# Kernel optimization log

Hardware: AMD Instinct MI355X
Metric: run time of the kernel (lower is better)

Reference implementation:

```python
import jax, jax.numpy as jnp
import numpy as np

B, N, E, EMB, IN = 8192, 100, 1600, 5, 1
MLP_IN = 50 * 2 * EMB + 50 * 52  # 3100


def _glorot(k, shape):
    fan_in = shape[0]
    return (jax.random.normal(k, shape, jnp.float32) / np.sqrt(fan_in)).astype(jnp.float32)


def setup_inputs() -> dict:
    key = jax.random.key(0)
    ks = jax.random.split(key, 32)
    inp = {
        "data": jax.random.normal(ks[0], (B, N, IN), jnp.float32),
        "d": jax.random.normal(ks[1], (B, 50, 52), jnp.float32),
        "src": jax.random.randint(ks[2], (E,), 0, N, jnp.int32),
        "dst": jax.random.randint(ks[3], (E,), 0, N, jnp.int32),
    }
    # 3 GatedRGCN layers: (1->5), (5->5), (5->5); each has a feature linear W,b and a gate linear G,gb
    dims = [(IN, EMB), (EMB, EMB), (EMB, EMB)]
    for i, (fi, fo) in enumerate(dims):
        inp[f"W{i}"] = _glorot(ks[4 + 4 * i], (fi, fo))
        inp[f"b{i}"] = jnp.zeros((fo,), jnp.float32)
        inp[f"G{i}"] = _glorot(ks[5 + 4 * i], (fo, fo))
        inp[f"gb{i}"] = jnp.zeros((fo,), jnp.float32)
    # MLP head: 3100 -> 128 -> 128 -> 64 -> 2
    mdims = [(MLP_IN, 128), (128, 128), (128, 64), (64, 2)]
    for i, (fi, fo) in enumerate(mdims):
        inp[f"F{i + 1}"] = _glorot(ks[16 + 2 * i], (fi, fo))
        inp[f"fb{i + 1}"] = jnp.zeros((fo,), jnp.float32)
    return inp


def _gated_rgcn_layer(h, src, dst, W, b, G, gb):
    # h: [B, N, F_in]; sum-aggregate neighbor features along edges, then gated linear.
    msgs = h[:, src, :]                                   # [B, E, F_in] gather
    agg = jnp.zeros_like(h).at[:, dst, :].add(msgs)       # [B, N, F_in] scatter-add
    h2 = agg @ W + b                                      # [B, N, F_out]
    gate = jax.nn.sigmoid(h2 @ G + gb)                    # elementwise edge-free gate
    return jax.nn.leaky_relu(gate * h2)                   # LeakyReLU(0.01), torch default


def reference(data, d, src, dst,
              W0, b0, G0, gb0, W1, b1, G1, gb1, W2, b2, G2, gb2,
              F1, fb1, F2, fb2, F3, fb3, F4, fb4):
    x = data
    x = _gated_rgcn_layer(x, src, dst, W0, b0, G0, gb0)
    x = _gated_rgcn_layer(x, src, dst, W1, b1, G1, gb1)
    x = _gated_rgcn_layer(x, src, dst, W2, b2, G2, gb2)
    x = x.reshape(x.shape[0], -1)                         # [B, 500]
    x = jnp.concatenate([x, d.reshape(d.shape[0], -1)], axis=1)  # [B, 3100]
    x = jax.nn.leaky_relu(x @ F1 + fb1)
    x = jax.nn.leaky_relu(x @ F2 + fb2)
    x = jax.nn.leaky_relu(x @ F3 + fb3)
    x = jax.nn.sigmoid(x @ F4 + fb4)                      # [B, 2]
    return x
```

## Files before the change

### kernel.cpp

```cpp
#include <hip/hip_runtime.h>
#include <math.h>

#define NT 256
#define NTG 1024
constexpr int B_   = 8192;
constexpr int N_   = 100;
constexpr int E_   = 1600;
constexpr int EMB  = 5;
constexpr int XDIM = 500;
constexpr int DDIM = 2600;
constexpr int XWP  = 512;
constexpr int DOFF = 512;
constexpr int KPAD = 3136;
constexpr int H1 = 128, H2 = 128, H3 = 64, HO = 2;

typedef short short8 __attribute__((ext_vector_type(8)));
typedef float f32x4  __attribute__((ext_vector_type(4)));

__device__ __forceinline__ float leaky(float v) { return v > 0.f ? v : 0.01f * v; }
__device__ __forceinline__ float sigm(float v)  { return 1.f / (1.f + __expf(-v)); }
__device__ __forceinline__ unsigned short f2bf(float f) {
  unsigned int x = __float_as_uint(f);
  return (unsigned short)((x + 0x7fffu + ((x >> 16) & 1u)) >> 16);
}

__global__ __launch_bounds__(NT) void setup_kernel(
    const int* __restrict__ src, const int* __restrict__ dst,
    int* __restrict__ off_g, int* __restrict__ lst_g,
    const float* __restrict__ F1, const float* __restrict__ F2, const float* __restrict__ F3,
    unsigned short* __restrict__ F1T, unsigned short* __restrict__ F2T, unsigned short* __restrict__ F3T,
    const float* __restrict__ dmat, unsigned short* __restrict__ aw)
{
  const int blk = blockIdx.x;
  const int t   = threadIdx.x;

  if (blk == 0) {
    __shared__ int cnt[N_ + 1];
    __shared__ int cur[N_];
    if (t <= N_) cnt[t] = 0;
    __syncthreads();
    for (int e = t; e < E_; e += NT) atomicAdd(&cnt[dst[e] + 1], 1);
    __syncthreads();
    if (t == 0) {
      int s = 0;
      for (int n = 0; n <= N_; ++n) { s += cnt[n]; cnt[n] = s; }
    }
    __syncthreads();
    if (t < N_) cur[t] = cnt[t];
    if (t <= N_) off_g[t] = cnt[t];
    __syncthreads();
    for (int e = t; e < E_; e += NT) {
      int d = dst[e];
      int p = atomicAdd(&cur[d], 1);
      lst_g[p] = src[e];
    }
  } else if (blk <= 320) {
    const int b = blk - 1;
    if (b < 128) {
      for (int k = t; k < KPAD; k += NT) {
        float v = 0.f;
        if (k < XDIM)                          v = F1[(size_t)k * H1 + b];
        else if (k >= DOFF && k < DOFF + DDIM) v = F1[(size_t)(k - DOFF + XDIM) * H1 + b];
        F1T[(size_t)b * KPAD + k] = f2bf(v);
      }
    } else if (b < 256) {
      int n = b - 128;
      if (t < 128) F2T[n * 128 + t] = f2bf(F2[(size_t)t * H2 + n]);
    } else {
      int n = b - 256;
      if (n < 64 && t < 128) F3T[n * 128 + t] = f2bf(F3[(size_t)t * H3 + n]);
    }
  } else {
    const int row = blk - 321;
    const float* dr = dmat + (size_t)row * DDIM;
    unsigned short* ar = aw + (size_t)row * KPAD + DOFF;
    for (int g = t; g < (KPAD - DOFF) / 8; g += NT) {
      uint4 p;
      if (g < DDIM / 8) {
        float4 f0 = *(const float4*)(dr + g * 8);
        float4 f1 = *(const float4*)(dr + g * 8 + 4);
        p.x = (__float_as_uint(f0.y) & 0xffff0000u) | (__float_as_uint(f0.x) >> 16);
        p.y = (__float_as_uint(f0.w) & 0xffff0000u) | (__float_as_uint(f0.z) >> 16);
        p.z = (__float_as_uint(f1.y) & 0xffff0000u) | (__float_as_uint(f1.x) >> 16);
        p.w = (__float_as_uint(f1.w) & 0xffff0000u) | (__float_as_uint(f1.z) >> 16);
      } else {
        p = make_uint4(0u, 0u, 0u, 0u);
      }
      *(uint4*)(ar + g * 8) = p;
    }
  }
}

constexpr int BT2 = 32;

__device__ __forceinline__ void rgcn_layer(
    const float* __restrict__ RB, float* __restrict__ WB,
    const float* __restrict__ wts, const int* __restrict__ soff,
    const int* __restrict__ sl160, int t, int wof)
{
  if (t < N_ * (BT2 / 4)) {
    const int n  = t >> 3;
    const int b4 = (t & 7) * 4;
    f32x4 a[5];
#pragma unroll
    for (int j = 0; j < 5; ++j) a[j] = (f32x4){0.f, 0.f, 0.f, 0.f};
    const int qe = soff[n + 1];
    for (int q = soff[n]; q < qe; ++q) {
      const float* base = RB + sl160[q] + b4;
#pragma unroll
      for (int j = 0; j < 5; ++j) a[j] += *(const f32x4*)(base + j * 32);
    }
    f32x4 h2[5];
#pragma unroll
    for (int j = 0; j < 5; ++j) {
      float bb = wts[wof + 25 + j];
      f32x4 v = (f32x4){bb, bb, bb, bb};
#pragma unroll
      for (int k = 0; k < 5; ++k) v += a[k] * wts[wof + k * 5 + j];
      h2[j] = v;
    }
#pragma unroll
    for (int j = 0; j < 5; ++j) {
      float gb = wts[wof + 55 + j];
      f32x4 g = (f32x4){gb, gb, gb, gb};
#pragma unroll
      for (int k = 0; k < 5; ++k) g += h2[k] * wts[wof + 30 + k * 5 + j];
      f32x4 o;
#pragma unroll
      for (int c = 0; c < 4; ++c) o[c] = leaky(sigm(g[c]) * h2[j][c]);
      *(f32x4*)(WB + n * 160 + j * 32 + b4) = o;
    }
  }
}

__global__ __launch_bounds__(NTG) void gnn_kernel(
    const float* __restrict__ data,
    const int* __restrict__ off_g, const int* __restrict__ lst_g,
    const float* __restrict__ W0, const float* __restrict__ b0, const float* __restrict__ G0, const float* __restrict__ gb0,
    const float* __restrict__ W1, const float* __restrict__ b1, const float* __restrict__ G1, const float* __restrict__ gb1,
    const float* __restrict__ W2, const float* __restrict__ b2, const float* __restrict__ G2, const float* __restrict__ gb2,
    unsigned short* __restrict__ aw)
{
  __shared__ __attribute__((aligned(16))) float bufA[BT2 * 513];
  __shared__ __attribute__((aligned(16))) float bufB[XDIM * BT2];
  __shared__ int   soff[N_ + 1];
  __shared__ int   sl160[E_];
  __shared__ float wts[160];
  const int t   = threadIdx.x;
  const int b0_ = blockIdx.x * BT2;

  for (int i = t; i < E_; i += NTG) sl160[i] = lst_g[i] * 160;
  if (t <= N_) soff[t] = off_g[t];
  if (t < 5)  { wts[t] = W0[t]; wts[5 + t] = b0[t]; wts[35 + t] = gb0[t]; }
  if (t < 25) { wts[10 + t] = G0[t];
                wts[40 + t] = W1[t]; wts[70 + t]  = G1[t];
                wts[100 + t] = W2[t]; wts[130 + t] = G2[t]; }
  if (t < 5)  { wts[65 + t] = b1[t]; wts[95 + t]  = gb1[t];
                wts[125 + t] = b2[t]; wts[155 + t] = gb2[t]; }
  for (int i = t; i < N_ * BT2; i += NTG) {
    int b = i / N_, n = i - b * N_;
    bufA[n * 160 + b] = data[(size_t)b0_ * N_ + i];
  }
  __syncthreads();

  if (t < N_ * (BT2 / 4)) {
    const int n  = t >> 3;
    const int b4 = (t & 7) * 4;
    f32x4 a = (f32x4){0.f, 0.f, 0.f, 0.f};
    const int qe = soff[n + 1];
    for (int q = soff[n]; q < qe; ++q) a += *(const f32x4*)(bufA + sl160[q] + b4);
    f32x4 h2[5];
#pragma unroll
    for (int j = 0; j < 5; ++j) {
      float bb = wts[5 + j];
      h2[j] = a * wts[j] + (f32x4){bb, bb, bb, bb};
    }
#pragma unroll
    for (int j = 0; j < 5; ++j) {
      float gb = wts[35 + j];
      f32x4 g = (f32x4){gb, gb, gb, gb};
#pragma unroll
      for (int k = 0; k < 5; ++k) g += h2[k] * wts[10 + k * 5 + j];
      f32x4 o;
#pragma unroll
      for (int c = 0; c < 4; ++c) o[c] = leaky(sigm(g[c]) * h2[j][c]);
      *(f32x4*)(bufB + n * 160 + j * 32 + b4) = o;
    }
  }
  __syncthreads();

  rgcn_layer(bufB, bufA, wts, soff, sl160, t, 40);
  __syncthreads();
  rgcn_layer(bufA, bufB, wts, soff, sl160, t, 100);
  __syncthreads();

  for (int i = t; i < BT2 * XWP; i += NTG) {
    int b = i & 31, r = i >> 5;
    bufA[b * 513 + r] = (r < XDIM) ? bufB[r * 32 + b] : 0.f;
  }
  __syncthreads();

  for (int i = t; i < BT2 * (XWP / 8); i += NTG) {
    int r8 = i & 63, b = i >> 6;
    const float* sp = bufA + b * 513 + r8 * 8;
    uint4 p;
    p.x = (unsigned)f2bf(sp[0]) | ((unsigned)f2bf(sp[1]) << 16);
    p.y = (unsigned)f2bf(sp[2]) | ((unsigned)f2bf(sp[3]) << 16);
    p.z = (unsigned)f2bf(sp[4]) | ((unsigned)f2bf(sp[5]) << 16);
    p.w = (unsigned)f2bf(sp[6]) | ((unsigned)f2bf(sp[7]) << 16);
    ((uint4*)aw)[(size_t)(b0_ + b) * (KPAD / 8) + r8] = p;
  }
}

constexpr int MBG = 32;
constexpr int MB2 = 16;
constexpr int EST = 136;
constexpr int KSPLIT = 7;
constexpr int NCH = KPAD / 64;
constexpr int SC = 7;

__global__ __launch_bounds__(NT, 4) void mlp_main(
    const unsigned short* __restrict__ aw,
    const unsigned short* __restrict__ F1T, float* __restrict__ part)
{
  const int t     = threadIdx.x;
  const int rb    = blockIdx.x & 255;
  const int split = blockIdx.x >> 8;
  const int row0  = rb * MBG;
  const int lane  = t & 63;
  const int w     = t >> 6;
  const int quad  = lane >> 4;
  const int ln    = lane & 15;
  const int q8    = quad * 8;
  const int cbeg  = split * SC;
  const int cend  = cbeg + SC;

  const unsigned short* xa0 = aw + (size_t)(row0 + ln) * KPAD + q8;
  const unsigned short* xa1 = xa0 + (size_t)16 * KPAD;
  const unsigned short* bt0 = F1T + (size_t)(w * 32 + ln) * KPAD + q8;
  const unsigned short* bt1 = bt0 + (size_t)16 * KPAD;

#define LOADF(Ax, Bx, c)                                                       \
  {                                                                            \
    int k0_ = (c) * 64;                                                        \
    _Pragma("unroll")                                                          \
    for (int s_ = 0; s_ < 2; ++s_) {                                           \
      int kk_ = k0_ + s_ * 32;                                                 \
      Ax[s_][0] = *(const short8*)(xa0 + kk_);                                 \
      Ax[s_][1] = *(const short8*)(xa1 + kk_);                                 \
      Bx[s_][0] = *(const short8*)(bt0 + kk_);                                 \
      Bx[s_][1] = *(const short8*)(bt1 + kk_);                                 \
    }                                                                          \
  }

  f32x4 a00 = {0.f, 0.f, 0.f, 0.f};
  f32x4 a01 = {0.f, 0.f, 0.f, 0.f};
  f32x4 a10 = {0.f, 0.f, 0.f, 0.f};
  f32x4 a11 = {0.f, 0.f, 0.f, 0.f};
  short8 A0[2][2], A1[2][2], B0[2][2], B1[2][2];

  LOADF(A0, B0, cbeg)
  LOADF(A1, B1, cbeg + 1)
  for (int c = cbeg; c < cend; ++c) {
    if ((c - cbeg) & 1) {
#pragma unroll
      for (int s = 0; s < 2; ++s) {
        a00 = __builtin_amdgcn_mfma_f32_16x16x32_bf16(A1[s][0], B1[s][0], a00, 0, 0, 0);
        a01 = __builtin_amdgcn_mfma_f32_16x16x32_bf16(A1[s][0], B1[s][1], a01, 0, 0, 0);
        a10 = __builtin_amdgcn_mfma_f32_16x16x32_bf16(A1[s][1], B1[s][0], a10, 0, 0, 0);
        a11 = __builtin_amdgcn_mfma_f32_16x16x32_bf16(A1[s][1], B1[s][1], a11, 0, 0, 0);
      }
      if (c + 2 < cend) LOADF(A1, B1, c + 2)
    } else {
#pragma unroll
      for (int s = 0; s < 2; ++s) {
        a00 = __builtin_amdgcn_mfma_f32_16x16x32_bf16(A0[s][0], B0[s][0], a00, 0, 0, 0);
        a01 = __builtin_amdgcn_mfma_f32_16x16x32_bf16(A0[s][0], B0[s][1], a01, 0, 0, 0);
        a10 = __builtin_amdgcn_mfma_f32_16x16x32_bf16(A0[s][1], B0[s][0], a10, 0, 0, 0);
        a11 = __builtin_amdgcn_mfma_f32_16x16x32_bf16(A0[s][1], B0[s][1], a11, 0, 0, 0);
      }
      if (c + 2 < cend) LOADF(A0, B0, c + 2)
    }
  }
#undef LOADF

  const int col0 = w * 32 + ln;
  float* pp = part + ((size_t)split * B_ + row0) * H1;
#pragma unroll
  for (int r = 0; r < 4; ++r) {
    int m = quad * 4 + r;
    pp[m * H1 + col0]             = a00[r];
    pp[m * H1 + col0 + 16]        = a01[r];
    pp[(m + 16) * H1 + col0]      = a10[r];
    pp[(m + 16) * H1 + col0 + 16] = a11[r];
  }
}

__global__ __launch_bounds__(NT) void tail_kernel(
    const float* __restrict__ part, const float* __restrict__ fb1,
    const unsigned short* __restrict__ F2T, const float* __restrict__ fb2,
    const unsigned short* __restrict__ F3T, const float* __restrict__ fb3,
    const float* __restrict__ F4, const float* __restrict__ fb4,
    float* __restrict__ out)
{
  __shared__ __attribute__((aligned(16))) unsigned short sH[MB2 * EST];
  __shared__ float sh3[MB2 * 68];

  const int t    = threadIdx.x;
  const int row0 = blockIdx.x * MB2;
  const int lane = t & 63;
  const int w    = t >> 6;
  const int quad = lane >> 4;
  const int ln   = lane & 15;
  const int q8   = quad * 8;
  constexpr size_t PS = (size_t)B_ * H1;

  for (int i = t; i < MB2 * H1; i += NT) {
    int m = i >> 7, col = i & 127;
    size_t off = (size_t)(row0 + m) * H1 + col;
    float v = fb1[col];
#pragma unroll
    for (int s = 0; s < KSPLIT; ++s) v += part[s * PS + off];
    sH[m * EST + col] = f2bf(leaky(v));
  }
  __syncthreads();

  const int col0 = w * 32 + ln;
  f32x4 a20 = {0.f, 0.f, 0.f, 0.f};
  f32x4 a21 = {0.f, 0.f, 0.f, 0.f};
  {
    const unsigned short* g2a = F2T + (size_t)col0 * H2 + q8;
    const unsigned short* g2b = g2a + (size_t)16 * H2;
#pragma unroll
    for (int s = 0; s < 4; ++s) {
      short8 b0f = *(const short8*)(g2a + s * 32);
      short8 b1f = *(const short8*)(g2b + s * 32);
      short8 af  = *(const short8*)(sH + ln * EST + s * 32 + q8);
      a20 = __builtin_amdgcn_mfma_f32_16x16x32_bf16(af, b0f, a20, 0, 0, 0);
      a21 = __builtin_amdgcn_mfma_f32_16x16x32_bf16(af, b1f, a21, 0, 0, 0);
    }
  }
  __syncthreads();
  {
    float bb0 = fb2[col0], bb1 = fb2[col0 + 16];
#pragma unroll
    for (int r = 0; r < 4; ++r) {
      int m = quad * 4 + r;
      sH[m * EST + col0]      = f2bf(leaky(a20[r] + bb0));
      sH[m * EST + col0 + 16] = f2bf(leaky(a21[r] + bb1));
    }
  }
  __syncthreads();

  f32x4 a3 = {0.f, 0.f, 0.f, 0.f};
  {
    const unsigned short* g3 = F3T + (size_t)(w * 16 + ln) * H2 + q8;
#pragma unroll
    for (int s = 0; s < 4; ++s) {
      short8 bf = *(const short8*)(g3 + s * 32);
      short8 af = *(const short8*)(sH + ln * EST + s * 32 + q8);
      a3 = __builtin_amdgcn_mfma_f32_16x16x32_bf16(af, bf, a3, 0, 0, 0);
    }
  }
  {
    int col = w * 16 + ln;
    float bb = fb3[col];
#pragma unroll
    for (int r = 0; r < 4; ++r)
      sh3[(quad * 4 + r) * 68 + col] = leaky(a3[r] + bb);
  }
  __syncthreads();

  if (t < MB2 * HO) {
    int m = t >> 1, j = t & 1;
    float a = fb4[j];
#pragma unroll 8
    for (int k = 0; k < H3; ++k) a += sh3[m * 68 + k] * F4[k * HO + j];
    out[(size_t)(row0 + m) * HO + j] = sigm(a);
  }
}

extern "C" void kernel_launch(void* const* d_in, const int* in_sizes, int n_in,
                              void* d_out, int out_size, void* d_ws, size_t ws_size,
                              hipStream_t stream) {
  const float* data = (const float*)d_in[0];
  const float* dmat = (const float*)d_in[1];
  const int*   src  = (const int*)d_in[2];
  const int*   dst  = (const int*)d_in[3];
  const float* W0 = (const float*)d_in[4];  const float* b0 = (const float*)d_in[5];
  const float* G0 = (const float*)d_in[6];  const float* gb0 = (const float*)d_in[7];
  const float* W1 = (const float*)d_in[8];  const float* b1 = (const float*)d_in[9];
  const float* G1 = (const float*)d_in[10]; const float* gb1 = (const float*)d_in[11];
  const float* W2 = (const float*)d_in[12]; const float* b2 = (const float*)d_in[13];
  const float* G2 = (const float*)d_in[14]; const float* gb2 = (const float*)d_in[15];
  const float* F1 = (const float*)d_in[16]; const float* fb1 = (const float*)d_in[17];
  const float* F2 = (const float*)d_in[18]; const float* fb2 = (const float*)d_in[19];
  const float* F3 = (const float*)d_in[20]; const float* fb3 = (const float*)d_in[21];
  const float* F4 = (const float*)d_in[22]; const float* fb4 = (const float*)d_in[23];
  float* out = (float*)d_out;

  unsigned short* aw  = (unsigned short*)d_ws;
  unsigned short* F1T = aw + (size_t)B_ * KPAD;
  unsigned short* F2T = F1T + 128 * KPAD;
  unsigned short* F3T = F2T + 128 * 128;
  int* off_g = (int*)(F3T + 64 * 128);
  int* lst_g = off_g + 104;
  float* part = (float*)(lst_g + 1600);

  setup_kernel<<<1 + 320 + B_, NT, 0, stream>>>(src, dst, off_g, lst_g,
                                                F1, F2, F3, F1T, F2T, F3T,
                                                dmat, aw);
  gnn_kernel<<<B_ / BT2, NTG, 0, stream>>>(data, off_g, lst_g,
                                           W0, b0, G0, gb0,
                                           W1, b1, G1, gb1,
                                           W2, b2, G2, gb2, aw);
  mlp_main<<<(B_ / MBG) * KSPLIT, NT, 0, stream>>>(aw, F1T, part);
  tail_kernel<<<B_ / MB2, NT, 0, stream>>>(part, fb1, F2T, fb2,
                                           F3T, fb3, F4, fb4, out);
}
```

Baseline: 264.0 us.

## Pre-swizzle MLP operands into MFMA fragment order for coalesced loads

The activation matrix and F1 weights are now stored in a blocked layout where each 32-wide k-chunk for a 16-row group is laid out exactly as the MFMA lanes read it. Each wave fetch becomes one contiguous 1 KB segment instead of strided row reads. The d-matrix conversion is restaged through shared memory, with 16 rows per block and far fewer blocks, to write this layout. The cost is an extra LDS transpose pass and more complex indexing in setup and in the GNN epilogue.

New measurement: 253.6 us. 1.04x faster.

```diff
diff --git a/kernel.cpp b/kernel.cpp
--- a/kernel.cpp
+++ b/kernel.cpp
@@ -12,6 +12,7 @@
 constexpr int XWP  = 512;
 constexpr int DOFF = 512;
 constexpr int KPAD = 3136;
+constexpr int NKC  = 98;
 constexpr int H1 = 128, H2 = 128, H3 = 64, HO = 2;
 
 typedef short short8 __attribute__((ext_vector_type(8)));
@@ -24,12 +25,13 @@
   return (unsigned short)((x + 0x7fffu + ((x >> 16) & 1u)) >> 16);
 }
 
+
 __global__ __launch_bounds__(NT) void setup_kernel(
     const int* __restrict__ src, const int* __restrict__ dst,
     int* __restrict__ off_g, int* __restrict__ lst_g,
     const float* __restrict__ F1, const float* __restrict__ F2, const float* __restrict__ F3,
-    unsigned short* __restrict__ F1T, unsigned short* __restrict__ F2T, unsigned short* __restrict__ F3T,
-    const float* __restrict__ dmat, unsigned short* __restrict__ aw)
+    unsigned short* __restrict__ F1c, unsigned short* __restrict__ F2T, unsigned short* __restrict__ F3T,
+    const float* __restrict__ dmat, unsigned short* __restrict__ awf)
 {
   const int blk = blockIdx.x;
   const int t   = threadIdx.x;
@@ -61,7 +63,9 @@
         float v = 0.f;
         if (k < XDIM)                          v = F1[(size_t)k * H1 + b];
         else if (k >= DOFF && k < DOFF + DDIM) v = F1[(size_t)(k - DOFF + XDIM) * H1 + b];
-        F1T[(size_t)b * KPAD + k] = f2bf(v);
+        int kc = k >> 5, q = (k >> 3) & 3, e = k & 7;
+        int lane = (b & 15) + q * 16;
+        F1c[((size_t)(b >> 4) * NKC + kc) * 512 + lane * 8 + e] = f2bf(v);
       }
     } else if (b < 256) {
       int n = b - 128;
@@ -71,22 +75,34 @@
       if (n < 64 && t < 128) F3T[n * 128 + t] = f2bf(F3[(size_t)t * H3 + n]);
     }
   } else {
-    const int row = blk - 321;
-    const float* dr = dmat + (size_t)row * DDIM;
-    unsigned short* ar = aw + (size_t)row * KPAD + DOFF;
-    for (int g = t; g < (KPAD - DOFF) / 8; g += NT) {
-      uint4 p;
-      if (g < DDIM / 8) {
-        float4 f0 = *(const float4*)(dr + g * 8);
-        float4 f1 = *(const float4*)(dr + g * 8 + 4);
-        p.x = (__float_as_uint(f0.y) & 0xffff0000u) | (__float_as_uint(f0.x) >> 16);
-        p.y = (__float_as_uint(f0.w) & 0xffff0000u) | (__float_as_uint(f0.z) >> 16);
-        p.z = (__float_as_uint(f1.y) & 0xffff0000u) | (__float_as_uint(f1.x) >> 16);
-        p.w = (__float_as_uint(f1.w) & 0xffff0000u) | (__float_as_uint(f1.z) >> 16);
-      } else {
-        p = make_uint4(0u, 0u, 0u, 0u);
-      }
-      *(uint4*)(ar + g * 8) = p;
+    const int R = blk - 321;
+    __shared__ __attribute__((aligned(16))) unsigned short tile[16][520];
+    const float* dbase = dmat + (size_t)R * 16 * DDIM;
+    for (int ct = 0; ct < 6; ++ct) {
+      const int c0 = ct * 512;
+      if (ct == 5) {
+        for (int i = t; i < 16 * 520; i += NT) ((unsigned short*)tile)[i] = 0;
+        __syncthreads();
+      }
+      const int nc4 = (ct < 5) ? 128 : 10;
+      for (int i = t; i < 16 * nc4; i += NT) {
+        int r = i / nc4, c4 = i - r * nc4;
+        float4 f = *(const float4*)(dbase + (size_t)r * DDIM + c0 + c4 * 4);
+        unsigned short* tp = &tile[r][c4 * 4];
+        tp[0] = (unsigned short)(__float_as_uint(f.x) >> 16);
+        tp[1] = (unsigned short)(__float_as_uint(f.y) >> 16);
+        tp[2] = (unsigned short)(__float_as_uint(f.z) >> 16);
+        tp[3] = (unsigned short)(__float_as_uint(f.w) >> 16);
+      }
+      __syncthreads();
+      const int nkc = (ct < 5) ? 16 : 2;
+      for (int i = t; i < nkc * 64; i += NT) {
+        int kcL = i >> 6, lane = i & 63;
+        int r = lane & 15, q = lane >> 4;
+        uint4 p = *(const uint4*)&tile[r][kcL * 32 + q * 8];
+        ((uint4*)awf)[((size_t)R * NKC + 16 + ct * 16 + kcL) * 64 + lane] = p;
+      }
+      __syncthreads();
     }
   }
 }
@@ -139,7 +155,7 @@
     const float* __restrict__ W0, const float* __restrict__ b0, const float* __restrict__ G0, const float* __restrict__ gb0,
     const float* __restrict__ W1, const float* __restrict__ b1, const float* __restrict__ G1, const float* __restrict__ gb1,
     const float* __restrict__ W2, const float* __restrict__ b2, const float* __restrict__ G2, const float* __restrict__ gb2,
-    unsigned short* __restrict__ aw)
+    unsigned short* __restrict__ awf)
 {
   __shared__ __attribute__((aligned(16))) float bufA[BT2 * 513];
   __shared__ __attribute__((aligned(16))) float bufB[XDIM * BT2];
@@ -200,15 +216,21 @@
   }
   __syncthreads();
 
-  for (int i = t; i < BT2 * (XWP / 8); i += NTG) {
-    int r8 = i & 63, b = i >> 6;
-    const float* sp = bufA + b * 513 + r8 * 8;
-    uint4 p;
-    p.x = (unsigned)f2bf(sp[0]) | ((unsigned)f2bf(sp[1]) << 16);
-    p.y = (unsigned)f2bf(sp[2]) | ((unsigned)f2bf(sp[3]) << 16);
-    p.z = (unsigned)f2bf(sp[4]) | ((unsigned)f2bf(sp[5]) << 16);
-    p.w = (unsigned)f2bf(sp[6]) | ((unsigned)f2bf(sp[7]) << 16);
-    ((uint4*)aw)[(size_t)(b0_ + b) * (KPAD / 8) + r8] = p;
+  {
+    const int R0 = blockIdx.x * 2;
+    for (int i = t; i < 32 * 64; i += NTG) {
+      int f = i >> 6, lane = i & 63;
+      int h = f >> 4, kc = f & 15;
+      int b = h * 16 + (lane & 15);
+      int k0 = kc * 32 + (lane >> 4) * 8;
+      const float* sp = bufA + b * 513 + k0;
+      uint4 p;
+      p.x = (unsigned)f2bf(sp[0]) | ((unsigned)f2bf(sp[1]) << 16);
+      p.y = (unsigned)f2bf(sp[2]) | ((unsigned)f2bf(sp[3]) << 16);
+      p.z = (unsigned)f2bf(sp[4]) | ((unsigned)f2bf(sp[5]) << 16);
+      p.w = (unsigned)f2bf(sp[6]) | ((unsigned)f2bf(sp[7]) << 16);
+      ((uint4*)awf)[((size_t)(R0 + h) * NKC + kc) * 64 + lane] = p;
+    }
   }
 }
 
@@ -216,12 +238,11 @@
 constexpr int MB2 = 16;
 constexpr int EST = 136;
 constexpr int KSPLIT = 7;
-constexpr int NCH = KPAD / 64;
-constexpr int SC = 7;
+constexpr int SCC = 7;
 
 __global__ __launch_bounds__(NT, 4) void mlp_main(
-    const unsigned short* __restrict__ aw,
-    const unsigned short* __restrict__ F1T, float* __restrict__ part)
+    const unsigned short* __restrict__ awf,
+    const unsigned short* __restrict__ F1c, float* __restrict__ part)
 {
   const int t     = threadIdx.x;
   const int rb    = blockIdx.x & 255;
@@ -231,25 +252,22 @@
   const int w     = t >> 6;
   const int quad  = lane >> 4;
   const int ln    = lane & 15;
-  const int q8    = quad * 8;
-  const int cbeg  = split * SC;
-  const int cend  = cbeg + SC;
-
-  const unsigned short* xa0 = aw + (size_t)(row0 + ln) * KPAD + q8;
-  const unsigned short* xa1 = xa0 + (size_t)16 * KPAD;
-  const unsigned short* bt0 = F1T + (size_t)(w * 32 + ln) * KPAD + q8;
-  const unsigned short* bt1 = bt0 + (size_t)16 * KPAD;
+  const int kc0   = split * (2 * SCC);
+
+  const unsigned short* a0p = awf + (((size_t)(rb * 2 + 0) * NKC + kc0) * 64 + lane) * 8;
+  const unsigned short* a1p = awf + (((size_t)(rb * 2 + 1) * NKC + kc0) * 64 + lane) * 8;
+  const unsigned short* b0p = F1c + (((size_t)(w * 2 + 0) * NKC + kc0) * 64 + lane) * 8;
+  const unsigned short* b1p = F1c + (((size_t)(w * 2 + 1) * NKC + kc0) * 64 + lane) * 8;
 
 #define LOADF(Ax, Bx, c)                                                       \
   {                                                                            \
-    int k0_ = (c) * 64;                                                        \
     _Pragma("unroll")                                                          \
     for (int s_ = 0; s_ < 2; ++s_) {                                           \
-      int kk_ = k0_ + s_ * 32;                                                 \
-      Ax[s_][0] = *(const short8*)(xa0 + kk_);                                 \
-      Ax[s_][1] = *(const short8*)(xa1 + kk_);                                 \
-      Bx[s_][0] = *(const short8*)(bt0 + kk_);                                 \
-      Bx[s_][1] = *(const short8*)(bt1 + kk_);                                 \
+      const int o_ = (2 * (c) + s_) * 512;                                     \
+      Ax[s_][0] = *(const short8*)(a0p + o_);                                  \
+      Ax[s_][1] = *(const short8*)(a1p + o_);                                  \
+      Bx[s_][0] = *(const short8*)(b0p + o_);                                  \
+      Bx[s_][1] = *(const short8*)(b1p + o_);                                  \
     }                                                                          \
   }
 
@@ -259,10 +277,10 @@
   f32x4 a11 = {0.f, 0.f, 0.f, 0.f};
   short8 A0[2][2], A1[2][2], B0[2][2], B1[2][2];
 
-  LOADF(A0, B0, cbeg)
-  LOADF(A1, B1, cbeg + 1)
-  for (int c = cbeg; c < cend; ++c) {
-    if ((c - cbeg) & 1) {
+  LOADF(A0, B0, 0)
+  LOADF(A1, B1, 1)
+  for (int c = 0; c < SCC; ++c) {
+    if (c & 1) {
 #pragma unroll
       for (int s = 0; s < 2; ++s) {
         a00 = __builtin_amdgcn_mfma_f32_16x16x32_bf16(A1[s][0], B1[s][0], a00, 0, 0, 0);
@@ -270,7 +288,7 @@
         a10 = __builtin_amdgcn_mfma_f32_16x16x32_bf16(A1[s][1], B1[s][0], a10, 0, 0, 0);
         a11 = __builtin_amdgcn_mfma_f32_16x16x32_bf16(A1[s][1], B1[s][1], a11, 0, 0, 0);
       }
-      if (c + 2 < cend) LOADF(A1, B1, c + 2)
+      if (c + 2 < SCC) LOADF(A1, B1, c + 2)
     } else {
 #pragma unroll
       for (int s = 0; s < 2; ++s) {
@@ -279,7 +297,7 @@
         a10 = __builtin_amdgcn_mfma_f32_16x16x32_bf16(A0[s][1], B0[s][0], a10, 0, 0, 0);
         a11 = __builtin_amdgcn_mfma_f32_16x16x32_bf16(A0[s][1], B0[s][1], a11, 0, 0, 0);
       }
-      if (c + 2 < cend) LOADF(A0, B0, c + 2)
+      if (c + 2 < SCC) LOADF(A0, B0, c + 2)
     }
   }
 #undef LOADF
@@ -399,22 +417,22 @@
   const float* F4 = (const float*)d_in[22]; const float* fb4 = (const float*)d_in[23];
   float* out = (float*)d_out;
 
-  unsigned short* aw  = (unsigned short*)d_ws;
-  unsigned short* F1T = aw + (size_t)B_ * KPAD;
-  unsigned short* F2T = F1T + 128 * KPAD;
+  unsigned short* awf = (unsigned short*)d_ws;
+  unsigned short* F1c = awf + (size_t)B_ * KPAD;
+  unsigned short* F2T = F1c + 128 * KPAD;
   unsigned short* F3T = F2T + 128 * 128;
   int* off_g = (int*)(F3T + 64 * 128);
   int* lst_g = off_g + 104;
   float* part = (float*)(lst_g + 1600);
 
-  setup_kernel<<<1 + 320 + B_, NT, 0, stream>>>(src, dst, off_g, lst_g,
-                                                F1, F2, F3, F1T, F2T, F3T,
-                                                dmat, aw);
+  setup_kernel<<<1 + 320 + 512, NT, 0, stream>>>(src, dst, off_g, lst_g,
+                                                 F1, F2, F3, F1c, F2T, F3T,
+                                                 dmat, awf);
   gnn_kernel<<<B_ / BT2, NTG, 0, stream>>>(data, off_g, lst_g,
                                            W0, b0, G0, gb0,
                                            W1, b1, G1, gb1,
-                                           W2, b2, G2, gb2, aw);
-  mlp_main<<<(B_ / MBG) * KSPLIT, NT, 0, stream>>>(aw, F1T, part);
+                                           W2, b2, G2, gb2, awf);
+  mlp_main<<<(B_ / MBG) * KSPLIT, NT, 0, stream>>>(awf, F1c, part);
   tail_kernel<<<B_ / MB2, NT, 0, stream>>>(part, fb1, F2T, fb2,
                                            F3T, fb3, F4, fb4, out);
 }
```
